# Performance work log

Hardware: AMD Instinct MI355X
Metric: run time of the kernel (lower is better)

## Reference

```python
import jax, jax.numpy as jnp
import numpy as np

NUM_HEADS = 16

def setup_inputs() -> dict:
    key = jax.random.key(0)
    ks = jax.random.split(key, 6)
    NH, S, K = 64, 1024, 64  # batch*heads, seq, head_dim
    H = NUM_HEADS
    max_seq_len = 2048
    return {
        "queries": jax.random.normal(ks[0], (NH, S, K), jnp.float32),
        "keys": jax.random.normal(ks[1], (NH, S, K), jnp.float32),
        "values": jax.random.normal(ks[2], (NH, S, K), jnp.float32),
        "u_bias": jax.random.normal(ks[3], (1, H, 1, K), jnp.float32),
        "v_bias": jax.random.normal(ks[4], (1, H, 1, K), jnp.float32),
        "R": jax.random.normal(ks[5], (H, max_seq_len, K), jnp.float32),
    }

def _rel_shift(pos_score):
    # Transformer-XL circular shift trick. pos_score: (NH, S, S_kv)
    NH, S, S_kv = pos_score.shape
    zero_pad = jnp.zeros((NH, S, 1), pos_score.dtype)
    padded = jnp.concatenate([zero_pad, pos_score], axis=-1)  # (NH, S, S_kv+1)
    padded = padded.reshape(NH, S_kv + 1, S)
    return padded[:, 1:, :].reshape(NH, S, S_kv)

def reference(queries, keys, values, u_bias, v_bias, R):
    H = NUM_HEADS
    NH, S, K = queries.shape
    N = NH // H
    S_kv = keys.shape[1]
    q = queries * (K ** -0.5)
    q = q.reshape(N, H, S, K)
    q_u = (q + u_bias).reshape(NH, S, K)
    q_v = (q + v_bias).reshape(NH, S, K)
    Rr = jnp.tile(R[:, :S_kv, :], (N, 1, 1))  # (NH, S_kv, K)
    content_score = jnp.einsum('bsk,btk->bst', q_u, keys)
    pos_score = jnp.einsum('bsk,btk->bst', q_v, Rr)
    pos_score = _rel_shift(pos_score)
    attn_weights = jax.nn.softmax(content_score + pos_score, axis=-1)
    attn = jnp.einsum('bst,btv->bsv', attn_weights, values)
    return attn
```

## Files before the change

kernel.cpp:

```cpp
#include <hip/hip_runtime.h>

#define SEQ  1024
#define HD   64
#define QTB  128
#define NT   16
#define RING 192
#define PST  84
#define WSTR (16*PST)
#define FB   (8*WSTR)
#define L2E  1.44269504f

typedef __attribute__((ext_vector_type(8))) _Float16 f16x8;
typedef __attribute__((ext_vector_type(4))) _Float16 f16x4;
typedef __attribute__((ext_vector_type(2))) _Float16 f16x2;
typedef __attribute__((ext_vector_type(4))) float    f32x4;

#define MFMA16(a,b,c)  __builtin_amdgcn_mfma_f32_16x16x32_f16(a,b,c,0,0,0)
#define MFMA161(a,b,c) __builtin_amdgcn_mfma_f32_16x16x16f16(a,b,c,0,0,0)

__device__ __forceinline__ int sw(int row, int c) {
    return (row << 6) + (c ^ ((row & 7) << 3));
}
__device__ __forceinline__ float4 ld4(const float* p) { return *(const float4*)p; }
__device__ __forceinline__ f16x8 cvt8(float4 a, float4 b) {
    return (f16x8){(_Float16)a.x,(_Float16)a.y,(_Float16)a.z,(_Float16)a.w,
                   (_Float16)b.x,(_Float16)b.y,(_Float16)b.z,(_Float16)b.w};
}
__device__ __forceinline__ f16x8 biasf8(float4 qa, float4 qb, float4 ba, float4 bb) {
    return (f16x8){(_Float16)(fmaf(qa.x,0.125f,ba.x)*L2E),(_Float16)(fmaf(qa.y,0.125f,ba.y)*L2E),
                   (_Float16)(fmaf(qa.z,0.125f,ba.z)*L2E),(_Float16)(fmaf(qa.w,0.125f,ba.w)*L2E),
                   (_Float16)(fmaf(qb.x,0.125f,bb.x)*L2E),(_Float16)(fmaf(qb.y,0.125f,bb.y)*L2E),
                   (_Float16)(fmaf(qb.z,0.125f,bb.z)*L2E),(_Float16)(fmaf(qb.w,0.125f,bb.w)*L2E)};
}

__global__ __launch_bounds__(512, 4)
void rpsdpa8(const float* __restrict__ Q, const float* __restrict__ Km,
             const float* __restrict__ Vm, const float* __restrict__ UB,
             const float* __restrict__ VB, const float* __restrict__ Rm,
             float* __restrict__ O)
{
    __shared__ __attribute__((aligned(16))) _Float16 sK[64*64];
    __shared__ __attribute__((aligned(16))) _Float16 sVt[2][64*64];
    __shared__ __attribute__((aligned(16))) _Float16 sR[RING*64];
    __shared__ __attribute__((aligned(16))) _Float16 sPT[FB + PST];
    __shared__ __attribute__((aligned(16))) _Float16 sQx[64];

    const int tid  = threadIdx.x;
    const int wv   = tid >> 6;
    const int lane = tid & 63;
    const int q    = lane & 15;
    const int G    = lane >> 4;

    const int bid = blockIdx.x;
    const int x   = bid & 7;
    const int y   = bid >> 3;
    const int h   = x + ((y & 1) << 3);
    const int n   = (y >> 1) & 3;
    const int bh  = n * 16 + h;
    const int i0  = (y >> 3) * QTB;

    const float* Qb = Q  + (size_t)bh * SEQ * HD;
    const float* Kb = Km + (size_t)bh * SEQ * HD;
    const float* Vb = Vm + (size_t)bh * SEQ * HD;
    const float* Rh = Rm + (size_t)h * 2048 * HD;

    f16x8 qu0, qu1, qvf0, qvf1;
    {
        const float* qr = Qb + (size_t)(i0 + 16*wv + q) * HD;
        const float* ub = UB + h * HD;
        const float* vb = VB + h * HD;
        {   int c = 8*G;
            float4 qa = ld4(qr+c), qb2 = ld4(qr+c+4);
            qu0  = biasf8(qa,qb2, ld4(ub+c), ld4(ub+c+4));
            qvf0 = biasf8(qa,qb2, ld4(vb+c), ld4(vb+c+4)); }
        {   int c = 32 + 8*G;
            float4 qa = ld4(qr+c), qb2 = ld4(qr+c+4);
            qu1  = biasf8(qa,qb2, ld4(ub+c), ld4(ub+c+4));
            qvf1 = biasf8(qa,qb2, ld4(vb+c), ld4(vb+c+4)); }
    }
    if (tid < 16) {
        int c0 = tid * 4;
        float4 v = make_float4(0.f,0.f,0.f,0.f);
        if (i0 + 128 < SEQ) {
            float4 q4 = ld4(Qb + (size_t)(i0+128)*HD + c0);
            float4 b4 = ld4(VB + h*HD + c0);
            v = make_float4(fmaf(q4.x,0.125f,b4.x)*L2E, fmaf(q4.y,0.125f,b4.y)*L2E,
                            fmaf(q4.z,0.125f,b4.z)*L2E, fmaf(q4.w,0.125f,b4.w)*L2E);
        }
        *(f16x4*)&sQx[c0] = (f16x4){(_Float16)v.x,(_Float16)v.y,(_Float16)v.z,(_Float16)v.w};
    }
    const int rK  = tid >> 3;
    const int cK  = (tid & 7) * 8;
    const int kp2 = (tid & 31) * 2;
    const int d0v = (tid >> 5) * 4;
    {
        const float* s = Kb + (size_t)rK*HD + cK;
        *(f16x8*)&sK[sw(rK, cK)] = cvt8(ld4(s), ld4(s+4));
    }
    {
        const float* sA = Vb + (size_t)kp2*HD + d0v;
        float4 a = ld4(sA), b2 = ld4(sA + HD);
        _Float16* vt = sVt[0];
        *(f16x2*)&vt[sw(d0v+0, kp2)] = (f16x2){(_Float16)a.x,(_Float16)b2.x};
        *(f16x2*)&vt[sw(d0v+1, kp2)] = (f16x2){(_Float16)a.y,(_Float16)b2.y};
        *(f16x2*)&vt[sw(d0v+2, kp2)] = (f16x2){(_Float16)a.z,(_Float16)b2.z};
        *(f16x2*)&vt[sw(d0v+3, kp2)] = (f16x2){(_Float16)a.w,(_Float16)b2.w};
    }
#pragma unroll 1
    for (int p = 0; p < 3; ++p) {
        int d = -i0 - 127 + p*64 + rK;
        int row = (d <= 0) ? (1023 + d) : ((d >= 2) ? d - 2 : 0);
        int slot = (d + 1536) % RING;
        const float* s = Rh + (size_t)row*HD + cK;
        *(f16x8*)&sR[sw(slot, cK)] = cvt8(ld4(s), ld4(s+4));
    }
    __syncthreads();

    int sbase = ((-i0 - 16*wv - 15) + 1536) % RING;
    float m_run = -3.0e38f, l_run = 0.f, corr = 0.f;
    f32x4 o0 = {}, o1 = {}, o2 = {}, o3 = {};
    f16x4 wfa0 = {}, wfa1 = {}, wfa2 = {}, wfa3 = {};

#pragma unroll 1
    for (int t = 0; t < NT; ++t) {
        const int j0 = t * 64;
        __builtin_amdgcn_s_setprio(1);
        f32x4 c0 = {}, c1 = {}, c2 = {}, c3 = {};
        {
            int cc = 8*G;
            c0 = MFMA16(*(const f16x8*)&sK[sw( 0+q, cc)], qu0, c0);
            c1 = MFMA16(*(const f16x8*)&sK[sw(16+q, cc)], qu0, c1);
            c2 = MFMA16(*(const f16x8*)&sK[sw(32+q, cc)], qu0, c2);
            c3 = MFMA16(*(const f16x8*)&sK[sw(48+q, cc)], qu0, c3);
            cc = 32 + 8*G;
            c0 = MFMA16(*(const f16x8*)&sK[sw( 0+q, cc)], qu1, c0);
            c1 = MFMA16(*(const f16x8*)&sK[sw(16+q, cc)], qu1, c1);
            c2 = MFMA16(*(const f16x8*)&sK[sw(32+q, cc)], qu1, c2);
            c3 = MFMA16(*(const f16x8*)&sK[sw(48+q, cc)], qu1, c3);
        }
        f32x4 p0 = {}, p1 = {}, p2 = {}, p3 = {}, p4 = {};
        {
            int r0 = sbase + q;       if (r0 >= RING) r0 -= RING;
            int r1 = sbase + 16 + q;  if (r1 >= RING) r1 -= RING;
            int r2 = sbase + 32 + q;  if (r2 >= RING) r2 -= RING;
            int r3 = sbase + 48 + q;  if (r3 >= RING) r3 -= RING;
            int r4 = sbase + 64 + q;  if (r4 >= RING) r4 -= RING;
            int cc = 8*G;
            p0 = MFMA16(*(const f16x8*)&sR[sw(r0, cc)], qvf0, p0);
            p1 = MFMA16(*(const f16x8*)&sR[sw(r1, cc)], qvf0, p1);
            p2 = MFMA16(*(const f16x8*)&sR[sw(r2, cc)], qvf0, p2);
            p3 = MFMA16(*(const f16x8*)&sR[sw(r3, cc)], qvf0, p3);
            p4 = MFMA16(*(const f16x8*)&sR[sw(r4, cc)], qvf0, p4);
            cc = 32 + 8*G;
            p0 = MFMA16(*(const f16x8*)&sR[sw(r0, cc)], qvf1, p0);
            p1 = MFMA16(*(const f16x8*)&sR[sw(r1, cc)], qvf1, p1);
            p2 = MFMA16(*(const f16x8*)&sR[sw(r2, cc)], qvf1, p2);
            p3 = MFMA16(*(const f16x8*)&sR[sw(r3, cc)], qvf1, p3);
            p4 = MFMA16(*(const f16x8*)&sR[sw(r4, cc)], qvf1, p4);
        }
        {
            _Float16* dst = &sPT[wv*WSTR + q*PST + 4*G];
            *(f16x4*)&dst[ 0] = (f16x4){(_Float16)p0[0],(_Float16)p0[1],(_Float16)p0[2],(_Float16)p0[3]};
            *(f16x4*)&dst[16] = (f16x4){(_Float16)p1[0],(_Float16)p1[1],(_Float16)p1[2],(_Float16)p1[3]};
            *(f16x4*)&dst[32] = (f16x4){(_Float16)p2[0],(_Float16)p2[1],(_Float16)p2[2],(_Float16)p2[3]};
            *(f16x4*)&dst[48] = (f16x4){(_Float16)p3[0],(_Float16)p3[1],(_Float16)p3[2],(_Float16)p3[3]};
            *(f16x4*)&dst[64] = (f16x4){(_Float16)p4[0],(_Float16)p4[1],(_Float16)p4[2],(_Float16)p4[3]};
        }
        if (wv == 7) {
            int sl = sbase + lane; if (sl >= RING) sl -= RING;
            float acc = 0.f;
#pragma unroll
            for (int c8 = 0; c8 < 8; ++c8) {
                f16x8 rv = *(const f16x8*)&sR[sw(sl, 8*c8)];
                f16x8 qx = *(const f16x8*)&sQx[8*c8];
#pragma unroll
                for (int e = 0; e < 8; ++e) acc = fmaf((float)rv[e], (float)qx[e], acc);
            }
            sPT[FB + 16 + lane] = (_Float16)acc;
        }
        if (t > 0) {
            float cg0 = __shfl(corr, 4*G + 0);
            float cg1 = __shfl(corr, 4*G + 1);
            float cg2 = __shfl(corr, 4*G + 2);
            float cg3 = __shfl(corr, 4*G + 3);
            f32x4 cg = {cg0, cg1, cg2, cg3};
            o0 *= cg; o1 *= cg; o2 *= cg; o3 *= cg;
            const _Float16* vt = sVt[(t-1) & 1];
#define PV_STEP(KB, A) { \
            o0 = MFMA161(A, *(const f16x4*)&vt[sw( 0+q, 16*KB+4*G)], o0); \
            o1 = MFMA161(A, *(const f16x4*)&vt[sw(16+q, 16*KB+4*G)], o1); \
            o2 = MFMA161(A, *(const f16x4*)&vt[sw(32+q, 16*KB+4*G)], o2); \
            o3 = MFMA161(A, *(const f16x4*)&vt[sw(48+q, 16*KB+4*G)], o3); }
            PV_STEP(0, wfa0) PV_STEP(1, wfa1) PV_STEP(2, wfa2) PV_STEP(3, wfa3)
        }
        __builtin_amdgcn_s_setprio(0);
        __syncthreads();
        {
            const int ii = i0 + 16*wv + q - j0;
            const int b1 = wv*WSTR + q*PST + 15 + 4*G - q;
            const int b2 = b1 + PST + ((q == 15) ? 16 : 0);
            float sc[16];
#pragma unroll
            for (int t4 = 0; t4 < 4; ++t4) {
#pragma unroll
                for (int r = 0; r < 4; ++r) {
                    const int off = r + 16*t4;
                    const int jrel = 4*G + off;
                    const float v1 = (float)sPT[b1 + off];
                    const float v2 = (float)sPT[b2 + off];
                    const int dj = jrel - ii;
                    const float add = (dj <= 0) ? v1 : ((dj == 1) ? 0.f : v2);
                    const float cv = (t4 == 0) ? c0[r] : (t4 == 1) ? c1[r] : (t4 == 2) ? c2[r] : c3[r];
                    sc[4*t4 + r] = cv + add;
                }
            }
            float mA = fmaxf(fmaxf(fmaxf(sc[0],sc[1]),fmaxf(sc[2],sc[3])),
                             fmaxf(fmaxf(sc[4],sc[5]),fmaxf(sc[6],sc[7])));
            float mB = fmaxf(fmaxf(fmaxf(sc[8],sc[9]),fmaxf(sc[10],sc[11])),
                             fmaxf(fmaxf(sc[12],sc[13]),fmaxf(sc[14],sc[15])));
            float mx = fmaxf(mA, mB);
            mx = fmaxf(mx, __shfl_xor(mx, 16));
            mx = fmaxf(mx, __shfl_xor(mx, 32));
            const float mnew = fmaxf(m_run, mx);
            corr = exp2f(m_run - mnew);
            m_run = mnew;
#pragma unroll
            for (int i = 0; i < 16; ++i) sc[i] = exp2f(sc[i] - mnew);
            float sA2 = ((sc[0]+sc[1])+(sc[2]+sc[3])) + ((sc[4]+sc[5])+(sc[6]+sc[7]));
            float sB2 = ((sc[8]+sc[9])+(sc[10]+sc[11])) + ((sc[12]+sc[13])+(sc[14]+sc[15]));
            float ssum = sA2 + sB2;
            ssum += __shfl_xor(ssum, 16);
            ssum += __shfl_xor(ssum, 32);
            l_run = l_run * corr + ssum;
            wfa0 = (f16x4){(_Float16)sc[0], (_Float16)sc[1], (_Float16)sc[2], (_Float16)sc[3]};
            wfa1 = (f16x4){(_Float16)sc[4], (_Float16)sc[5], (_Float16)sc[6], (_Float16)sc[7]};
            wfa2 = (f16x4){(_Float16)sc[8], (_Float16)sc[9], (_Float16)sc[10],(_Float16)sc[11]};
            wfa3 = (f16x4){(_Float16)sc[12],(_Float16)sc[13],(_Float16)sc[14],(_Float16)sc[15]};
            if (t + 1 < NT) {
                const float* s = Kb + (size_t)(j0 + 64 + rK)*HD + cK;
                float4 ka = ld4(s), kb = ld4(s+4);
                const float* sA = Vb + (size_t)(j0 + 64 + kp2)*HD + d0v;
                float4 va = ld4(sA), vb2 = ld4(sA + HD);
                int d = j0 - i0 + 65 + rK;
                int row = (d <= 0) ? (1023 + d) : ((d >= 2) ? d - 2 : 0);
                const float* sr = Rh + (size_t)row*HD + cK;
                float4 ra = ld4(sr), rb = ld4(sr+4);
                *(f16x8*)&sK[sw(rK, cK)] = cvt8(ka, kb);
                _Float16* vt = sVt[(t+1) & 1];
                *(f16x2*)&vt[sw(d0v+0, kp2)] = (f16x2){(_Float16)va.x,(_Float16)vb2.x};
                *(f16x2*)&vt[sw(d0v+1, kp2)] = (f16x2){(_Float16)va.y,(_Float16)vb2.y};
                *(f16x2*)&vt[sw(d0v+2, kp2)] = (f16x2){(_Float16)va.z,(_Float16)vb2.z};
                *(f16x2*)&vt[sw(d0v+3, kp2)] = (f16x2){(_Float16)va.w,(_Float16)vb2.w};
                int slot = (d + 1536) % RING;
                *(f16x8*)&sR[sw(slot, cK)] = cvt8(ra, rb);
            }
            sbase += 64; if (sbase >= RING) sbase -= RING;
        }
        __syncthreads();
    }
    {
        float cg0 = __shfl(corr, 4*G + 0);
        float cg1 = __shfl(corr, 4*G + 1);
        float cg2 = __shfl(corr, 4*G + 2);
        float cg3 = __shfl(corr, 4*G + 3);
        f32x4 cg = {cg0, cg1, cg2, cg3};
        o0 *= cg; o1 *= cg; o2 *= cg; o3 *= cg;
        const _Float16* vt = sVt[(NT-1) & 1];
        PV_STEP(0, wfa0) PV_STEP(1, wfa1) PV_STEP(2, wfa2) PV_STEP(3, wfa3)
#undef PV_STEP
    }
    {
        float i0v = 1.f / __shfl(l_run, 4*G + 0);
        float i1v = 1.f / __shfl(l_run, 4*G + 1);
        float i2v = 1.f / __shfl(l_run, 4*G + 2);
        float i3v = 1.f / __shfl(l_run, 4*G + 3);
        f32x4 inv = {i0v, i1v, i2v, i3v};
#pragma unroll
        for (int reg = 0; reg < 4; ++reg) {
            size_t base = ((size_t)bh*SEQ + i0 + 16*wv + 4*G + reg) * HD + q;
            O[base +  0] = o0[reg] * inv[reg];
            O[base + 16] = o1[reg] * inv[reg];
            O[base + 32] = o2[reg] * inv[reg];
            O[base + 48] = o3[reg] * inv[reg];
        }
    }
}

extern "C" void kernel_launch(void* const* d_in, const int* in_sizes, int n_in,
                              void* d_out, int out_size, void* d_ws, size_t ws_size,
                              hipStream_t stream) {
    const float* Q  = (const float*)d_in[0];
    const float* K  = (const float*)d_in[1];
    const float* V  = (const float*)d_in[2];
    const float* UB = (const float*)d_in[3];
    const float* VB = (const float*)d_in[4];
    const float* R  = (const float*)d_in[5];
    float* O = (float*)d_out;

    rpsdpa8<<<dim3(512), dim3(512), 0, stream>>>(Q, K, V, UB, VB, R, O);
}
```

Before: 83.22 us.

## Add lazy softmax rescaling, defer row-sum reduction, and hoist next-tile global loads

Uses a wave-wide ballot so the running max and accumulator rescale are updated only when some row's max grows by more than a threshold of 8 (log2 units). Otherwise the stale max is kept and the o-register scaling is skipped. Per-lane partial row sums are accumulated and cross-lane reduced once at the end, removing shuffles from the loop. Next-tile K/V/R global loads are issued before the softmax so their latency overlaps it, and the R ring slot is tracked incrementally. Launch bounds drop to 2 waves per SIMD, which lets each thread use more registers but may lower occupancy. The threshold lets exp values reach up to 2^8, which adds fp16 range risk for the probabilities.

```diff
diff --git a/kernel.cpp b/kernel.cpp
--- a/kernel.cpp
+++ b/kernel.cpp
@@ -33,11 +33,11 @@
                    (_Float16)(fmaf(qb.z,0.125f,bb.z)*L2E),(_Float16)(fmaf(qb.w,0.125f,bb.w)*L2E)};
 }
 
-__global__ __launch_bounds__(512, 4)
-void rpsdpa8(const float* __restrict__ Q, const float* __restrict__ Km,
-             const float* __restrict__ Vm, const float* __restrict__ UB,
-             const float* __restrict__ VB, const float* __restrict__ Rm,
-             float* __restrict__ O)
+__global__ __launch_bounds__(512, 2)
+void rpsdpa11(const float* __restrict__ Q, const float* __restrict__ Km,
+              const float* __restrict__ Vm, const float* __restrict__ UB,
+              const float* __restrict__ VB, const float* __restrict__ Rm,
+              float* __restrict__ O)
 {
     __shared__ __attribute__((aligned(16))) _Float16 sK[64*64];
     __shared__ __attribute__((aligned(16))) _Float16 sVt[2][64*64];
@@ -117,7 +117,11 @@
     __syncthreads();
 
     int sbase = ((-i0 - 16*wv - 15) + 1536) % RING;
-    float m_run = -3.0e38f, l_run = 0.f, corr = 0.f;
+    int d_st    = -i0 + 65 + rK;
+    int slot_st = (d_st + 1536) % RING;
+
+    float m_run = -3.0e38f, l_part = 0.f, corr = 0.f;
+    int   sflag = 1;
     f32x4 o0 = {}, o1 = {}, o2 = {}, o3 = {};
     f16x4 wfa0 = {}, wfa1 = {}, wfa2 = {}, wfa3 = {};
 
@@ -179,12 +183,14 @@
             sPT[FB + 16 + lane] = (_Float16)acc;
         }
         if (t > 0) {
-            float cg0 = __shfl(corr, 4*G + 0);
-            float cg1 = __shfl(corr, 4*G + 1);
-            float cg2 = __shfl(corr, 4*G + 2);
-            float cg3 = __shfl(corr, 4*G + 3);
-            f32x4 cg = {cg0, cg1, cg2, cg3};
-            o0 *= cg; o1 *= cg; o2 *= cg; o3 *= cg;
+            if (sflag) {
+                float cg0 = __shfl(corr, 4*G + 0);
+                float cg1 = __shfl(corr, 4*G + 1);
+                float cg2 = __shfl(corr, 4*G + 2);
+                float cg3 = __shfl(corr, 4*G + 3);
+                f32x4 cg = {cg0, cg1, cg2, cg3};
+                o0 *= cg; o1 *= cg; o2 *= cg; o3 *= cg;
+            }
             const _Float16* vt = sVt[(t-1) & 1];
 #define PV_STEP(KB, A) { \
             o0 = MFMA161(A, *(const f16x4*)&vt[sw( 0+q, 16*KB+4*G)], o0); \
@@ -196,6 +202,16 @@
         __builtin_amdgcn_s_setprio(0);
         __syncthreads();
         {
+            float4 ka, kb, va, vb2, ra, rb;
+            if (t + 1 < NT) {
+                const float* s = Kb + (size_t)(j0 + 64 + rK)*HD + cK;
+                ka = ld4(s); kb = ld4(s+4);
+                const float* sA = Vb + (size_t)(j0 + 64 + kp2)*HD + d0v;
+                va = ld4(sA); vb2 = ld4(sA + HD);
+                int row = (d_st <= 0) ? (1023 + d_st) : ((d_st >= 2) ? d_st - 2 : 0);
+                const float* sr = Rh + (size_t)row*HD + cK;
+                ra = ld4(sr); rb = ld4(sr+4);
+            }
             const int ii = i0 + 16*wv + q - j0;
             const int b1 = wv*WSTR + q*PST + 15 + 4*G - q;
             const int b2 = b1 + PST + ((q == 15) ? 16 : 0);
@@ -221,59 +237,60 @@
             float mx = fmaxf(mA, mB);
             mx = fmaxf(mx, __shfl_xor(mx, 16));
             mx = fmaxf(mx, __shfl_xor(mx, 32));
-            const float mnew = fmaxf(m_run, mx);
-            corr = exp2f(m_run - mnew);
-            m_run = mnew;
-#pragma unroll
-            for (int i = 0; i < 16; ++i) sc[i] = exp2f(sc[i] - mnew);
+            if (__ballot(mx > m_run + 8.0f)) {
+                const float mnew = fmaxf(m_run, mx);
+                corr = exp2f(m_run - mnew);
+                m_run = mnew;
+                l_part *= corr;
+                sflag = 1;
+            } else {
+                sflag = 0;
+            }
+#pragma unroll
+            for (int i = 0; i < 16; ++i) sc[i] = exp2f(sc[i] - m_run);
             float sA2 = ((sc[0]+sc[1])+(sc[2]+sc[3])) + ((sc[4]+sc[5])+(sc[6]+sc[7]));
             float sB2 = ((sc[8]+sc[9])+(sc[10]+sc[11])) + ((sc[12]+sc[13])+(sc[14]+sc[15]));
-            float ssum = sA2 + sB2;
-            ssum += __shfl_xor(ssum, 16);
-            ssum += __shfl_xor(ssum, 32);
-            l_run = l_run * corr + ssum;
+            l_part += sA2 + sB2;
             wfa0 = (f16x4){(_Float16)sc[0], (_Float16)sc[1], (_Float16)sc[2], (_Float16)sc[3]};
             wfa1 = (f16x4){(_Float16)sc[4], (_Float16)sc[5], (_Float16)sc[6], (_Float16)sc[7]};
             wfa2 = (f16x4){(_Float16)sc[8], (_Float16)sc[9], (_Float16)sc[10],(_Float16)sc[11]};
             wfa3 = (f16x4){(_Float16)sc[12],(_Float16)sc[13],(_Float16)sc[14],(_Float16)sc[15]};
             if (t + 1 < NT) {
-                const float* s = Kb + (size_t)(j0 + 64 + rK)*HD + cK;
-                float4 ka = ld4(s), kb = ld4(s+4);
-                const float* sA = Vb + (size_t)(j0 + 64 + kp2)*HD + d0v;
-                float4 va = ld4(sA), vb2 = ld4(sA + HD);
-                int d = j0 - i0 + 65 + rK;
-                int row = (d <= 0) ? (1023 + d) : ((d >= 2) ? d - 2 : 0);
-                const float* sr = Rh + (size_t)row*HD + cK;
-                float4 ra = ld4(sr), rb = ld4(sr+4);
                 *(f16x8*)&sK[sw(rK, cK)] = cvt8(ka, kb);
                 _Float16* vt = sVt[(t+1) & 1];
                 *(f16x2*)&vt[sw(d0v+0, kp2)] = (f16x2){(_Float16)va.x,(_Float16)vb2.x};
                 *(f16x2*)&vt[sw(d0v+1, kp2)] = (f16x2){(_Float16)va.y,(_Float16)vb2.y};
                 *(f16x2*)&vt[sw(d0v+2, kp2)] = (f16x2){(_Float16)va.z,(_Float16)vb2.z};
                 *(f16x2*)&vt[sw(d0v+3, kp2)] = (f16x2){(_Float16)va.w,(_Float16)vb2.w};
-                int slot = (d + 1536) % RING;
-                *(f16x8*)&sR[sw(slot, cK)] = cvt8(ra, rb);
+                *(f16x8*)&sR[sw(slot_st, cK)] = cvt8(ra, rb);
+                d_st += 64;
+                slot_st += 64; if (slot_st >= RING) slot_st -= RING;
             }
             sbase += 64; if (sbase >= RING) sbase -= RING;
         }
         __syncthreads();
     }
     {
-        float cg0 = __shfl(corr, 4*G + 0);
-        float cg1 = __shfl(corr, 4*G + 1);
-        float cg2 = __shfl(corr, 4*G + 2);
-        float cg3 = __shfl(corr, 4*G + 3);
-        f32x4 cg = {cg0, cg1, cg2, cg3};
-        o0 *= cg; o1 *= cg; o2 *= cg; o3 *= cg;
+        if (sflag) {
+            float cg0 = __shfl(corr, 4*G + 0);
+            float cg1 = __shfl(corr, 4*G + 1);
+            float cg2 = __shfl(corr, 4*G + 2);
+            float cg3 = __shfl(corr, 4*G + 3);
+            f32x4 cg = {cg0, cg1, cg2, cg3};
+            o0 *= cg; o1 *= cg; o2 *= cg; o3 *= cg;
+        }
         const _Float16* vt = sVt[(NT-1) & 1];
         PV_STEP(0, wfa0) PV_STEP(1, wfa1) PV_STEP(2, wfa2) PV_STEP(3, wfa3)
 #undef PV_STEP
     }
     {
-        float i0v = 1.f / __shfl(l_run, 4*G + 0);
-        float i1v = 1.f / __shfl(l_run, 4*G + 1);
-        float i2v = 1.f / __shfl(l_run, 4*G + 2);
-        float i3v = 1.f / __shfl(l_run, 4*G + 3);
+        float l_tot = l_part;
+        l_tot += __shfl_xor(l_tot, 16);
+        l_tot += __shfl_xor(l_tot, 32);
+        float i0v = 1.f / __shfl(l_tot, 4*G + 0);
+        float i1v = 1.f / __shfl(l_tot, 4*G + 1);
+        float i2v = 1.f / __shfl(l_tot, 4*G + 2);
+        float i3v = 1.f / __shfl(l_tot, 4*G + 3);
         f32x4 inv = {i0v, i1v, i2v, i3v};
 #pragma unroll
         for (int reg = 0; reg < 4; ++reg) {
@@ -297,5 +314,5 @@
     const float* R  = (const float*)d_in[5];
     float* O = (float*)d_out;
 
-    rpsdpa8<<<dim3(512), dim3(512), 0, stream>>>(Q, K, V, UB, VB, R, O);
-}
+    rpsdpa11<<<dim3(512), dim3(512), 0, stream>>>(Q, K, V, UB, VB, R, O);
+}
```

Result: slower. 143.5 us (+72.5%).
